# Kernel tuning notes

Measured on AMD Instinct MI355X. Metric: run time of the kernel, lower is better.

The kernel has to match this reference:

```python
import jax, jax.numpy as jnp
import numpy as np

T, R, HEADS, H, L = 4, 8, 4, 128, 2
DK = H // HEADS
NPT = 25000
N = T * NPT
E = 600000
IN_DIMS = [512, 256, 128, 64]


def setup_inputs() -> dict:
    key = jax.random.key(0)
    ks = iter(jax.random.split(key, 64))
    d = {}
    # per-type raw node features (concatenation order = type order)
    for i, di in enumerate(IN_DIMS):
        d[f"nf{i}"] = jax.random.normal(next(ks), (NPT, di), jnp.float32)
    # per-type input encoder MLPs: Linear(di,256) -> ReLU -> Linear(256,H)
    for i, di in enumerate(IN_DIMS):
        d[f"enc_w1_{i}"] = jax.random.normal(next(ks), (di, 256), jnp.float32) * (1.0 / np.sqrt(di))
        d[f"enc_b1_{i}"] = jnp.zeros((256,), jnp.float32)
        d[f"enc_w2_{i}"] = jax.random.normal(next(ks), (256, H), jnp.float32) * (1.0 / np.sqrt(256))
        d[f"enc_b2_{i}"] = jnp.zeros((H,), jnp.float32)
    # HGT conv params, stacked over L layers
    sc = 1.0 / np.sqrt(H)
    for nm in ["Wk", "Wq", "Wv", "Wa"]:
        d[nm] = jax.random.normal(next(ks), (L, T, H, H), jnp.float32) * sc
        d["b" + nm[1]] = jnp.zeros((L, T, H), jnp.float32)
    eye = jnp.broadcast_to(jnp.eye(DK, dtype=jnp.float32), (L, R, HEADS, DK, DK))
    d["rel_att"] = eye + 0.05 * jax.random.normal(next(ks), (L, R, HEADS, DK, DK), jnp.float32)
    d["rel_msg"] = eye + 0.05 * jax.random.normal(next(ks), (L, R, HEADS, DK, DK), jnp.float32)
    d["rel_pri"] = jnp.ones((L, R, HEADS), jnp.float32)
    d["skip"] = jnp.zeros((L, T), jnp.float32)  # sigmoid(0)=0.5 gate
    d["gamma"] = jnp.ones((L, H), jnp.float32)
    d["beta"] = jnp.zeros((L, H), jnp.float32)
    # graph structure
    d["node_types"] = jnp.repeat(jnp.arange(T, dtype=jnp.int32), NPT)
    d["edge_index"] = jax.random.randint(next(ks), (2, E), 0, N, jnp.int32)
    d["edge_types"] = jax.random.randint(next(ks), (E,), 0, R, jnp.int32)
    return d


def typed_linear(x, nt, W, b):
    # W: [T,H,H], b: [T,H]; select per-node-type transform
    allt = jnp.einsum('nd,tdh->tnh', x, W) + b[:, None, :]  # [T,N,H]
    return allt[nt, jnp.arange(x.shape[0])]  # [N,H]


def layer_norm(x, g, b):
    m = x.mean(-1, keepdims=True)
    v = jnp.var(x, -1, keepdims=True)
    return (x - m) * jax.lax.rsqrt(v + 1e-5) * g + b


def hgt_layer(h, nt, src, dst, et, Wk, bk, Wq, bq, Wv, bv, Wa, ba, ra, rm, rp, skip, g, be):
    n = h.shape[0]
    k = typed_linear(h, nt, Wk, bk).reshape(n, HEADS, DK)
    q = typed_linear(h, nt, Wq, bq).reshape(n, HEADS, DK)
    v = typed_linear(h, nt, Wv, bv).reshape(n, HEADS, DK)
    k_s, v_s, q_d = k[src], v[src], q[dst]  # [E,HEADS,DK]
    # relation-conditioned key/message transforms (small fixed loop over R relations)
    kt = jnp.zeros_like(k_s)
    mt = jnp.zeros_like(v_s)
    for r in range(R):
        msk = (et == r)[:, None, None]
        kt = kt + jnp.where(msk, jnp.einsum('ehd,hdf->ehf', k_s, ra[r]), 0.0)
        mt = mt + jnp.where(msk, jnp.einsum('ehd,hdf->ehf', v_s, rm[r]), 0.0)
    att = (q_d * kt).sum(-1) * rp[et] * (1.0 / np.sqrt(DK))  # [E,HEADS]
    # segment softmax over incoming edges of each target node
    amax = jax.ops.segment_max(att, dst, num_segments=n)
    amax = jnp.where(jnp.isfinite(amax), amax, 0.0)
    ea = jnp.exp(att - amax[dst])
    den = jax.ops.segment_sum(ea, dst, num_segments=n)
    w = ea / jnp.maximum(den[dst], 1e-9)
    res = jax.ops.segment_sum(w[:, :, None] * mt, dst, num_segments=n).reshape(n, H)
    trans = typed_linear(jax.nn.gelu(res, approximate=False), nt, Wa, ba)
    alpha = jax.nn.sigmoid(skip)[nt][:, None]
    out = trans * alpha + h * (1.0 - alpha)
    return layer_norm(out, g, be)


def reference(nf0, nf1, nf2, nf3,
              enc_w1_0, enc_b1_0, enc_w2_0, enc_b2_0,
              enc_w1_1, enc_b1_1, enc_w2_1, enc_b2_1,
              enc_w1_2, enc_b1_2, enc_w2_2, enc_b2_2,
              enc_w1_3, enc_b1_3, enc_w2_3, enc_b2_3,
              Wk, bk, Wq, bq, Wv, bv, Wa, ba,
              rel_att, rel_msg, rel_pri, skip, gamma, beta,
              node_types, edge_index, edge_types):
    encs = [(enc_w1_0, enc_b1_0, enc_w2_0, enc_b2_0),
            (enc_w1_1, enc_b1_1, enc_w2_1, enc_b2_1),
            (enc_w1_2, enc_b1_2, enc_w2_2, enc_b2_2),
            (enc_w1_3, enc_b1_3, enc_w2_3, enc_b2_3)]
    embs = [jax.nn.relu(nf @ w1 + b1) @ w2 + b2
            for nf, (w1, b1, w2, b2) in zip([nf0, nf1, nf2, nf3], encs)]
    h = jnp.concatenate(embs, axis=0)  # [N,H]; dropout is identity in eval mode
    src, dst = edge_index[0], edge_index[1]
    for l in range(L):
        h = hgt_layer(h, node_types, src, dst, edge_types,
                      Wk[l], bk[l], Wq[l], bq[l], Wv[l], bv[l], Wa[l], ba[l],
                      rel_att[l], rel_msg[l], rel_pri[l], skip[l], gamma[l], beta[l])
    return h
```

## Files before the change

### kernel.cpp

```cpp
#include <hip/hip_runtime.h>
#include <math.h>


#define NPT   25000
#define NN    100000
#define EE    600000
#define HD    128
#define NRELS 8

typedef unsigned short u16;
typedef unsigned int   u32;
using s16x8 = __attribute__((ext_vector_type(8))) short;
using f32x4 = __attribute__((ext_vector_type(4))) float;

__device__ __forceinline__ u16 f2bf(float x){
  u32 u = __float_as_uint(x);
  u += 0x7fffu + ((u >> 16) & 1u);
  return (u16)(u >> 16);
}
__device__ __forceinline__ float bf2f(u16 v){ return __uint_as_float(((u32)v) << 16); }

struct CastArgs {
  const float* src[12];
  u16* dst[12];
  int K[12], N[12], B[12];
  int blk0[13];
};

__global__ __launch_bounds__(256) void cast_all(CastArgs a){
  int blk = blockIdx.x;
  int s = 0;
  while (s < 11 && blk >= a.blk0[s + 1]) s++;
  long idx = (long)(blk - a.blk0[s]) * 256 + threadIdx.x;
  int K = a.K[s], N = a.N[s];
  long per = (long)K * N;
  long tot = per * a.B[s];
  if (idx >= tot) return;
  int b = (int)(idx / per);
  long rem = idx - (long)b * per;
  int n = (int)(rem / K), k = (int)(rem - (long)n * K);
  a.dst[s][idx] = f2bf(a.src[s][(long)b * per + (long)k * N + n]);
}

__global__ __launch_bounds__(256) void pack_rel(const float* __restrict__ ra,
                                                const float* __restrict__ rm,
                                                u16* __restrict__ out){
  int idx = blockIdx.x * 256 + threadIdx.x;
  if (idx >= 131072) return;
  int j = idx & 7, lane = (idx >> 3) & 63, nc = (idx >> 9) & 1;
  int h = (idx >> 10) & 3, r = (idx >> 12) & 7, mat = (idx >> 15) & 1, l = idx >> 16;
  const float* src = mat ? rm : ra;
  float v = src[(((long)l * 8 + r) * 4 + h) * 1024 + ((lane >> 4) * 8 + j) * 32 + nc * 16 + (lane & 15)];
  out[idx] = f2bf(v);
}

__global__ __launch_bounds__(256) void hist_key(const int* __restrict__ ei,
                                                const int* __restrict__ et,
                                                int* __restrict__ hist){
  int e = blockIdx.x * 256 + threadIdx.x;
  if (e < EE) atomicAdd(&hist[et[e] * NN + ei[EE + e]], 1);
}

__global__ __launch_bounds__(256) void scan_part_g(const int* __restrict__ in,
                                                   int* __restrict__ bsum, int n){
  __shared__ int sh[256];
  int i = blockIdx.x * 256 + threadIdx.x;
  sh[threadIdx.x] = (i < n) ? in[i] : 0;
  __syncthreads();
  for (int s = 128; s > 0; s >>= 1){
    if (threadIdx.x < s) sh[threadIdx.x] += sh[threadIdx.x + s];
    __syncthreads();
  }
  if (threadIdx.x == 0) bsum[blockIdx.x] = sh[0];
}

__global__ __launch_bounds__(512) void scan_bsum(int* bsum, int nb){
  __shared__ int sh[512];
  int t = threadIdx.x;
  int orig = (t < nb) ? bsum[t] : 0;
  sh[t] = orig;
  __syncthreads();
  for (int off = 1; off < 512; off <<= 1){
    int u = (t >= off) ? sh[t - off] : 0;
    __syncthreads();
    sh[t] += u;
    __syncthreads();
  }
  if (t < nb) bsum[t] = sh[t] - orig;
}

__global__ __launch_bounds__(256) void scan_fin_g(const int* __restrict__ in,
                                                  const int* __restrict__ bsum,
                                                  int* __restrict__ out, int n){
  __shared__ int sh[256];
  int i = blockIdx.x * 256 + threadIdx.x;
  int v = (i < n) ? in[i] : 0;
  sh[threadIdx.x] = v;
  __syncthreads();
  for (int off = 1; off < 256; off <<= 1){
    int u = (threadIdx.x >= off) ? sh[threadIdx.x - off] : 0;
    __syncthreads();
    sh[threadIdx.x] += u;
    __syncthreads();
  }
  if (i < n) out[i] = sh[threadIdx.x] - v + bsum[blockIdx.x];
}

__global__ void extract_offs(const int* __restrict__ cur, int* __restrict__ meta){
  int r = threadIdx.x;
  if (r < NRELS) meta[16 + r] = cur[r * NN];
  if (r == 0) meta[24] = EE;
}

__global__ __launch_bounds__(256) void scatter_key(const int* __restrict__ ei,
                                                   const int* __restrict__ et,
                                                   int* __restrict__ cur,
                                                   int* __restrict__ ss, int* __restrict__ sd){
  int e = blockIdx.x * 256 + threadIdx.x;
  if (e < EE){
    int s = ei[e], d = ei[EE + e];
    int p = atomicAdd(&cur[et[e] * NN + d], 1);
    ss[p] = s;
    sd[p] = d;
  }
}

__global__ __launch_bounds__(256) void hist_dst(const int* __restrict__ sd, int* __restrict__ hist){
  int e = blockIdx.x * 256 + threadIdx.x;
  if (e < EE) atomicAdd(&hist[sd[e]], 1);
}

__global__ __launch_bounds__(256) void scan_fin(const int* __restrict__ hist,
                                                const int* __restrict__ bsum,
                                                int* __restrict__ rowp, int* __restrict__ cursor){
  __shared__ int sh[256];
  int i = blockIdx.x * 256 + threadIdx.x;
  int v = (i < NN) ? hist[i] : 0;
  sh[threadIdx.x] = v;
  __syncthreads();
  for (int off = 1; off < 256; off <<= 1){
    int u = (threadIdx.x >= off) ? sh[threadIdx.x - off] : 0;
    __syncthreads();
    sh[threadIdx.x] += u;
    __syncthreads();
  }
  int excl = sh[threadIdx.x] - v + bsum[blockIdx.x];
  if (i < NN){ rowp[i] = excl; cursor[i] = excl; }
  if (i == NN - 1) rowp[NN] = excl + v;
}

__global__ __launch_bounds__(256) void dp_scat(const int* __restrict__ sd,
                                               int* __restrict__ cursor, int* __restrict__ dp){
  int e = blockIdx.x * 256 + threadIdx.x;
  if (e < EE) dp[e] = atomicAdd(&cursor[sd[e]], 1);
}

template<bool A_F32, bool RELU, bool OUTF32, bool OUTBF16>
__global__ __launch_bounds__(256)
void gemm_k(const void* __restrict__ Ap, const u16* __restrict__ Bt,
            const float* __restrict__ bias,
            float* __restrict__ Cf, u16* __restrict__ Cbf,
            int M, int N, int K, int sAr, int sB, int sBias, int sCr,
            int ldC, int colOff)
{
  __shared__ __align__(16) u16 As[128 * 40];
  __shared__ __align__(16) u16 Bs[128 * 40];
  int z = blockIdx.z;
  int tid = threadIdx.x, wv = tid >> 6, lane = tid & 63;
  int m0 = blockIdx.x * 128, n0 = blockIdx.y * 128;
  int wm = (wv >> 1) * 64, wn = (wv & 1) * 64;
  long aBase = (long)z * sAr * K;
  const u16*   Ab  = (const u16*)Ap;
  const float* Afp = (const float*)Ap;
  const u16* Bz = Bt + (long)z * sB;
  const float* biz = bias + (long)z * sBias;
  long cRow0 = (long)z * sCr;
  int r2 = tid >> 1, hf = tid & 1;

  f32x4 acc[4][4];
  #pragma unroll
  for (int i = 0; i < 4; i++)
    #pragma unroll
    for (int j = 0; j < 4; j++) acc[i][j] = (f32x4){0.f, 0.f, 0.f, 0.f};

  for (int kk = 0; kk < K; kk += 32){
    {
      int gm = m0 + r2;
      #pragma unroll
      for (int c = 0; c < 2; c++){
        int ko = kk + c * 16 + hf * 8;
        union { u16 us[8]; uint4 v; } pk;
        if (gm < M){
          if (!A_F32){
            pk.v = *(const uint4*)(Ab + aBase + (long)gm * K + ko);
          } else {
            const float* s = Afp + aBase + (long)gm * K + ko;
            float4 f0 = *(const float4*)s;
            float4 f1 = *(const float4*)(s + 4);
            pk.us[0] = f2bf(f0.x); pk.us[1] = f2bf(f0.y); pk.us[2] = f2bf(f0.z); pk.us[3] = f2bf(f0.w);
            pk.us[4] = f2bf(f1.x); pk.us[5] = f2bf(f1.y); pk.us[6] = f2bf(f1.z); pk.us[7] = f2bf(f1.w);
          }
        } else {
          pk.v = make_uint4(0u, 0u, 0u, 0u);
        }
        *(uint4*)&As[r2 * 40 + c * 16 + hf * 8] = pk.v;
      }
    }
    {
      int gn = n0 + r2;
      #pragma unroll
      for (int c = 0; c < 2; c++){
        int ko = kk + c * 16 + hf * 8;
        uint4 v;
        if (gn < N) v = *(const uint4*)(Bz + (long)gn * K + ko);
        else        v = make_uint4(0u, 0u, 0u, 0u);
        *(uint4*)&Bs[r2 * 40 + c * 16 + hf * 8] = v;
      }
    }
    __syncthreads();
    s16x8 af[4], bfr[4];
    int rr = lane & 15, q8 = (lane >> 4) * 8;
    #pragma unroll
    for (int mt = 0; mt < 4; mt++) af[mt]  = *(const s16x8*)&As[(wm + mt * 16 + rr) * 40 + q8];
    #pragma unroll
    for (int nt = 0; nt < 4; nt++) bfr[nt] = *(const s16x8*)&Bs[(wn + nt * 16 + rr) * 40 + q8];
    #pragma unroll
    for (int mt = 0; mt < 4; mt++)
      #pragma unroll
      for (int nt = 0; nt < 4; nt++)
        acc[mt][nt] = __builtin_amdgcn_mfma_f32_16x16x32_bf16(af[mt], bfr[nt], acc[mt][nt], 0, 0, 0);
    __syncthreads();
  }
  int col = lane & 15, row4 = (lane >> 4) * 4;
  #pragma unroll
  for (int mt = 0; mt < 4; mt++){
    #pragma unroll
    for (int nt = 0; nt < 4; nt++){
      int gn = n0 + wn + nt * 16 + col;
      float bb = (gn < N) ? biz[gn] : 0.f;
      #pragma unroll
      for (int r = 0; r < 4; r++){
        int gm = m0 + wm + mt * 16 + row4 + r;
        if (gm < M && gn < N){
          float vv = acc[mt][nt][r] + bb;
          if (RELU) vv = fmaxf(vv, 0.f);
          long ci = (cRow0 + gm) * (long)ldC + colOff + gn;
          if (OUTF32)  Cf[ci]  = vv;
          if (OUTBF16) Cbf[ci] = f2bf(vv);
        }
      }
    }
  }
}

__global__ __launch_bounds__(256)
void gemm_kvq(const u16* __restrict__ A,
              const u16* __restrict__ BK, const u16* __restrict__ BV, const u16* __restrict__ BQ,
              const float* __restrict__ bK, const float* __restrict__ bV, const float* __restrict__ bQ,
              u16* __restrict__ kvb, u16* __restrict__ qb)
{
  __shared__ __align__(16) u16 As[128 * 40];
  __shared__ __align__(16) u16 Bs[128 * 40];
  int bx = blockIdx.x;
  int grp = bx % 3;
  int m0 = (bx / 3) * 128;
  int z = blockIdx.z;
  int tid = threadIdx.x, wv = tid >> 6, lane = tid & 63;
  int wm = (wv >> 1) * 64, wn = (wv & 1) * 64;
  long aBase = (long)z * NPT * 128;
  const u16* Bz = ((grp == 0) ? BK : (grp == 1) ? BV : BQ) + (long)z * 16384;
  const float* biz = ((grp == 0) ? bK : (grp == 1) ? bV : bQ) + z * 128;
  u16* C = (grp == 2) ? qb : kvb;
  int ldC = (grp == 2) ? 128 : 256;
  int colOff = (grp == 1) ? 128 : 0;
  long cRow0 = (long)z * NPT;
  int r2 = tid >> 1, hf = tid & 1;

  f32x4 acc[4][4];
  #pragma unroll
  for (int i = 0; i < 4; i++)
    #pragma unroll
    for (int j = 0; j < 4; j++) acc[i][j] = (f32x4){0.f, 0.f, 0.f, 0.f};

  for (int kk = 0; kk < 128; kk += 32){
    {
      int gm = m0 + r2;
      #pragma unroll
      for (int c = 0; c < 2; c++){
        int ko = kk + c * 16 + hf * 8;
        uint4 v;
        if (gm < NPT) v = *(const uint4*)(A + aBase + (long)gm * 128 + ko);
        else          v = make_uint4(0u, 0u, 0u, 0u);
        *(uint4*)&As[r2 * 40 + c * 16 + hf * 8] = v;
      }
    }
    {
      int gn = r2;
      #pragma unroll
      for (int c = 0; c < 2; c++){
        int ko = kk + c * 16 + hf * 8;
        uint4 v = *(const uint4*)(Bz + (long)gn * 128 + ko);
        *(uint4*)&Bs[r2 * 40 + c * 16 + hf * 8] = v;
      }
    }
    __syncthreads();
    s16x8 af[4], bfr[4];
    int rr = lane & 15, q8 = (lane >> 4) * 8;
    #pragma unroll
    for (int mt = 0; mt < 4; mt++) af[mt]  = *(const s16x8*)&As[(wm + mt * 16 + rr) * 40 + q8];
    #pragma unroll
    for (int nt = 0; nt < 4; nt++) bfr[nt] = *(const s16x8*)&Bs[(wn + nt * 16 + rr) * 40 + q8];
    #pragma unroll
    for (int mt = 0; mt < 4; mt++)
      #pragma unroll
      for (int nt = 0; nt < 4; nt++)
        acc[mt][nt] = __builtin_amdgcn_mfma_f32_16x16x32_bf16(af[mt], bfr[nt], acc[mt][nt], 0, 0, 0);
    __syncthreads();
  }
  int col = lane & 15, row4 = (lane >> 4) * 4;
  #pragma unroll
  for (int mt = 0; mt < 4; mt++){
    #pragma unroll
    for (int nt = 0; nt < 4; nt++){
      int gn = wn + nt * 16 + col;
      float bb = biz[gn];
      #pragma unroll
      for (int r = 0; r < 4; r++){
        int gm = m0 + wm + mt * 16 + row4 + r;
        if (gm < NPT){
          float vv = acc[mt][nt][r] + bb;
          C[(cRow0 + gm) * (long)ldC + colOff + gn] = f2bf(vv);
        }
      }
    }
  }
}

__global__ __launch_bounds__(256)
void gemm_ln(const u16* __restrict__ A, const u16* __restrict__ Bt,
             const float* __restrict__ bias,
             float* __restrict__ h, u16* __restrict__ hb,
             const float* __restrict__ skl, const float* __restrict__ gmv,
             const float* __restrict__ btv)
{
  __shared__ __align__(16) u16 As[128 * 40];
  __shared__ __align__(16) u16 Bs[128 * 40];
  __shared__ float red[128][4];
  int z = blockIdx.z;
  int tid = threadIdx.x, wv = tid >> 6, lane = tid & 63;
  int m0 = blockIdx.x * 128;
  int wm = (wv >> 1) * 64, wn = (wv & 1) * 64;
  long aBase = (long)z * NPT * 128;
  const u16* Bz = Bt + (long)z * 16384;
  const float* biz = bias + z * 128;
  int r2 = tid >> 1, hf = tid & 1;

  f32x4 acc[4][4];
  #pragma unroll
  for (int i = 0; i < 4; i++)
    #pragma unroll
    for (int j = 0; j < 4; j++) acc[i][j] = (f32x4){0.f, 0.f, 0.f, 0.f};

  for (int kk = 0; kk < 128; kk += 32){
    {
      int gm = m0 + r2;
      #pragma unroll
      for (int c = 0; c < 2; c++){
        int ko = kk + c * 16 + hf * 8;
        uint4 v;
        if (gm < NPT) v = *(const uint4*)(A + aBase + (long)gm * 128 + ko);
        else          v = make_uint4(0u, 0u, 0u, 0u);
        *(uint4*)&As[r2 * 40 + c * 16 + hf * 8] = v;
      }
    }
    {
      int gn = r2;
      #pragma unroll
      for (int c = 0; c < 2; c++){
        int ko = kk + c * 16 + hf * 8;
        uint4 v = *(const uint4*)(Bz + (long)gn * 128 + ko);
        *(uint4*)&Bs[r2 * 40 + c * 16 + hf * 8] = v;
      }
    }
    __syncthreads();
    s16x8 af[4], bfr[4];
    int rr = lane & 15, q8 = (lane >> 4) * 8;
    #pragma unroll
    for (int mt = 0; mt < 4; mt++) af[mt]  = *(const s16x8*)&As[(wm + mt * 16 + rr) * 40 + q8];
    #pragma unroll
    for (int nt = 0; nt < 4; nt++) bfr[nt] = *(const s16x8*)&Bs[(wn + nt * 16 + rr) * 40 + q8];
    #pragma unroll
    for (int mt = 0; mt < 4; mt++)
      #pragma unroll
      for (int nt = 0; nt < 4; nt++)
        acc[mt][nt] = __builtin_amdgcn_mfma_f32_16x16x32_bf16(af[mt], bfr[nt], acc[mt][nt], 0, 0, 0);
    __syncthreads();
  }

  int col = lane & 15, q = lane >> 4, row4 = q * 4;
  float alpha = 1.f / (1.f + __expf(-skl[z]));
  float bb[4], ga[4], be[4];
  #pragma unroll
  for (int nt = 0; nt < 4; nt++){
    int gn = wn + nt * 16 + col;
    bb[nt] = biz[gn];
    ga[nt] = gmv[gn];
    be[nt] = btv[gn];
  }

  #pragma unroll
  for (int mt = 0; mt < 4; mt++){
    #pragma unroll
    for (int rr = 0; rr < 4; rr++){
      int gmr = m0 + wm + mt * 16 + row4 + rr;
      bool ok = gmr < NPT;
      long rb = ((long)z * NPT + gmr) * HD;
      float p1 = 0.f, p2 = 0.f;
      #pragma unroll
      for (int nt = 0; nt < 4; nt++){
        int gn = wn + nt * 16 + col;
        float hv = ok ? h[rb + gn] : 0.f;
        float vf = (acc[mt][nt][rr] + bb[nt]) * alpha + hv * (1.f - alpha);
        acc[mt][nt][rr] = vf;
        p1 += vf;
        p2 += vf * vf;
      }
      #pragma unroll
      for (int mk = 1; mk < 16; mk <<= 1){
        p1 += __shfl_xor(p1, mk);
        p2 += __shfl_xor(p2, mk);
      }
      if (col == 0){
        int lr = wm + mt * 16 + row4 + rr;
        red[lr][2 * (wn >> 6)]     = p1;
        red[lr][2 * (wn >> 6) + 1] = p2;
      }
    }
  }
  __syncthreads();

  #pragma unroll
  for (int mt = 0; mt < 4; mt++){
    #pragma unroll
    for (int rr = 0; rr < 4; rr++){
      int lr = wm + mt * 16 + row4 + rr;
      int gmr = m0 + lr;
      float ts1 = red[lr][0] + red[lr][2];
      float ts2 = red[lr][1] + red[lr][3];
      float mean = ts1 * (1.f / HD);
      float var = ts2 * (1.f / HD) - mean * mean;
      float rstd = rsqrtf(fmaxf(var, 0.f) + 1e-5f);
      if (gmr < NPT){
        long rb = ((long)z * NPT + gmr) * HD;
        #pragma unroll
        for (int nt = 0; nt < 4; nt++){
          int gn = wn + nt * 16 + col;
          float y = (acc[mt][nt][rr] - mean) * rstd * ga[nt] + be[nt];
          h[rb + gn]  = y;
          hb[rb + gn] = f2bf(y);
        }
      }
    }
  }
}

__global__ __launch_bounds__(256)
void edge_fused(const u16* __restrict__ kvb, const u16* __restrict__ qb,
                const int* __restrict__ ss, const int* __restrict__ sd,
                const int* __restrict__ dp, const int* __restrict__ offs,
                const u16* __restrict__ relpk, const float* __restrict__ rp,
                float* __restrict__ att, u16* __restrict__ wt, int l)
{
  __shared__ __align__(16) u16 ktS[4][16][136];
  int r = blockIdx.y;
  int lo = offs[r], hi = offs[r + 1];
  int base = lo + blockIdx.x * 64;
  if (base >= hi) return;
  int cnt = hi - base; if (cnt > 64) cnt = 64;
  int tid = threadIdx.x, wv = tid >> 6, lane = tid & 63;
  if (wv * 16 >= cnt) return;
  int wcnt = cnt - wv * 16; if (wcnt > 16) wcnt = 16;
  int m = lane & 15, g = lane >> 4;
  int ebase = base + wv * 16;

  int mq = lane >> 2, part = lane & 3;
  int mqc = (mq < wcnt) ? mq : (wcnt - 1);
  int dnq = sd[ebase + mqc];
  int dpq = dp[ebase + mqc];
  const u16* qrow = qb + (long)dnq * 128 + part * 32;
  uint4 qv[4];
  #pragma unroll
  for (int j = 0; j < 4; j++) qv[j] = *(const uint4*)(qrow + j * 8);

  int mm = (m < wcnt) ? m : (wcnt - 1);
  int s_ = ss[ebase + mm];
  const u16* krow = kvb + (long)s_ * 256;
  s16x8 ak[4], av[4];
  #pragma unroll
  for (int h = 0; h < 4; h++){
    ak[h] = *(const s16x8*)(krow + h * 32 + g * 8);
    av[h] = *(const s16x8*)(krow + 128 + h * 32 + g * 8);
  }

  const u16* relA = relpk + (((long)l * 2) * 8 + r) * 4096;
  f32x4 tt[4][2];
  #pragma unroll
  for (int h = 0; h < 4; h++)
    #pragma unroll
    for (int nc = 0; nc < 2; nc++){
      s16x8 b = *(const s16x8*)(relA + h * 1024 + nc * 512 + lane * 8);
      tt[h][nc] = __builtin_amdgcn_mfma_f32_16x16x32_bf16(ak[h], b, (f32x4){0.f,0.f,0.f,0.f}, 0, 0, 0);
    }
  int col = lane & 15, row4 = (lane >> 4) * 4;
  #pragma unroll
  for (int h = 0; h < 4; h++)
    #pragma unroll
    for (int nc = 0; nc < 2; nc++)
      #pragma unroll
      for (int rr = 0; rr < 4; rr++)
        ktS[wv][row4 + rr][h * 32 + nc * 16 + col] = f2bf(tt[h][nc][rr]);
  __asm__ volatile("s_waitcnt lgkmcnt(0)" ::: "memory");

  {
    const u16* ktrow = &ktS[wv][mq][part * 32];
    float p = 0.f;
    #pragma unroll
    for (int j = 0; j < 4; j++){
      uint4 kk4 = *(const uint4*)(ktrow + j * 8);
      uint4 qq4 = qv[j];
      const u32* kw = (const u32*)&kk4;
      const u32* qw = (const u32*)&qq4;
      #pragma unroll
      for (int t = 0; t < 4; t++){
        u32 kk = kw[t], qq = qw[t];
        p = fmaf(bf2f((u16)(kk & 0xffffu)), bf2f((u16)(qq & 0xffffu)), p);
        p = fmaf(__uint_as_float(kk & 0xffff0000u), __uint_as_float(qq & 0xffff0000u), p);
      }
    }
    if (mq < wcnt)
      att[(long)dpq * 4 + part] = p * rp[r * 4 + part] * 0.17677669529663689f;
  }
  __asm__ volatile("s_waitcnt lgkmcnt(0)" ::: "memory");

  const u16* relM = relpk + (((long)l * 2 + 1) * 8 + r) * 4096;
  #pragma unroll
  for (int h = 0; h < 4; h++)
    #pragma unroll
    for (int nc = 0; nc < 2; nc++){
      s16x8 b = *(const s16x8*)(relM + h * 1024 + nc * 512 + lane * 8);
      tt[h][nc] = __builtin_amdgcn_mfma_f32_16x16x32_bf16(av[h], b, (f32x4){0.f,0.f,0.f,0.f}, 0, 0, 0);
    }
  #pragma unroll
  for (int h = 0; h < 4; h++)
    #pragma unroll
    for (int nc = 0; nc < 2; nc++)
      #pragma unroll
      for (int rr = 0; rr < 4; rr++)
        ktS[wv][row4 + rr][h * 32 + nc * 16 + col] = f2bf(tt[h][nc][rr]);
  __asm__ volatile("s_waitcnt lgkmcnt(0)" ::: "memory");

  if (mq < wcnt){
    #pragma unroll
    for (int j = 0; j < 4; j++){
      uint4 v = *(const uint4*)&ktS[wv][mq][part * 32 + j * 8];
      *(uint4*)(wt + (long)dpq * 128 + part * 32 + j * 8) = v;
    }
  }
}

__global__ __launch_bounds__(256)
void seg_reduce(const float* __restrict__ att, const u16* __restrict__ wt,
                const int* __restrict__ rowp, u16* __restrict__ gA)
{
  __shared__ __align__(16) float eas[4][64][4];
  int wv = threadIdx.x >> 6, lane = threadIdx.x & 63;
  int d = blockIdx.x * 4 + wv;
  if (d >= NN) return;
  int first = rowp[d], last = rowp[d + 1];
  int hsel = lane >> 4;
  float m0 = -1e30f, m1 = -1e30f, m2 = -1e30f, m3 = -1e30f;
  float den0 = 0, den1 = 0, den2 = 0, den3 = 0;
  float acc0 = 0, acc1 = 0;
  for (int c0 = first; c0 < last; c0 += 64){
    int cnt = min(64, last - c0);
    float4 a;
    if (lane < cnt) a = *(const float4*)(att + (long)(c0 + lane) * 4);
    else            a = make_float4(-1e30f, -1e30f, -1e30f, -1e30f);
    float c_0 = a.x, c_1 = a.y, c_2 = a.z, c_3 = a.w;
    #pragma unroll
    for (int mm = 1; mm < 64; mm <<= 1){
      c_0 = fmaxf(c_0, __shfl_xor(c_0, mm));
      c_1 = fmaxf(c_1, __shfl_xor(c_1, mm));
      c_2 = fmaxf(c_2, __shfl_xor(c_2, mm));
      c_3 = fmaxf(c_3, __shfl_xor(c_3, mm));
    }
    float n0 = fmaxf(m0, c_0), n1 = fmaxf(m1, c_1), n2 = fmaxf(m2, c_2), n3 = fmaxf(m3, c_3);
    float r0 = __expf(m0 - n0), r1 = __expf(m1 - n1), r2 = __expf(m2 - n2), r3 = __expf(m3 - n3);
    den0 *= r0; den1 *= r1; den2 *= r2; den3 *= r3;
    float rsel = (hsel == 0) ? r0 : (hsel == 1) ? r1 : (hsel == 2) ? r2 : r3;
    acc0 *= rsel; acc1 *= rsel;
    m0 = n0; m1 = n1; m2 = n2; m3 = n3;
    float e_0 = 0, e_1 = 0, e_2 = 0, e_3 = 0;
    if (lane < cnt){
      e_0 = __expf(a.x - m0); e_1 = __expf(a.y - m1);
      e_2 = __expf(a.z - m2); e_3 = __expf(a.w - m3);
    }
    float s0 = e_0, s1 = e_1, s2 = e_2, s3 = e_3;
    #pragma unroll
    for (int mm = 1; mm < 64; mm <<= 1){
      s0 += __shfl_xor(s0, mm); s1 += __shfl_xor(s1, mm);
      s2 += __shfl_xor(s2, mm); s3 += __shfl_xor(s3, mm);
    }
    den0 += s0; den1 += s1; den2 += s2; den3 += s3;
    *(float4*)&eas[wv][lane][0] = make_float4(e_0, e_1, e_2, e_3);
    for (int i = 0; i < cnt; i++){
      float ea = eas[wv][i][hsel];
      u32 w = *(const u32*)(wt + (long)(c0 + i) * HD + 2 * lane);
      acc0 = fmaf(ea, bf2f((u16)(w & 0xffffu)), acc0);
      acc1 = fmaf(ea, __uint_as_float(w & 0xffff0000u), acc1);
    }
  }
  float dh = (hsel == 0) ? den0 : (hsel == 1) ? den1 : (hsel == 2) ? den2 : den3;
  float x0 = acc0 / fmaxf(dh, 1e-9f);
  float x1 = acc1 / fmaxf(dh, 1e-9f);
  x0 = 0.5f * x0 * (1.0f + erff(x0 * 0.70710678118654752f));
  x1 = 0.5f * x1 * (1.0f + erff(x1 * 0.70710678118654752f));
  u32 o = (u32)f2bf(x0) | ((u32)f2bf(x1) << 16);
  *(u32*)(gA + (long)d * HD + 2 * lane) = o;
}

extern "C" void kernel_launch(void* const* d_in, const int* in_sizes, int n_in,
                              void* d_out, int out_size, void* d_ws, size_t ws_size,
                              hipStream_t stream)
{
  const float* nf[4]  = {(const float*)d_in[0], (const float*)d_in[1], (const float*)d_in[2], (const float*)d_in[3]};
  const float* ew1[4] = {(const float*)d_in[4], (const float*)d_in[8],  (const float*)d_in[12], (const float*)d_in[16]};
  const float* eb1[4] = {(const float*)d_in[5], (const float*)d_in[9],  (const float*)d_in[13], (const float*)d_in[17]};
  const float* ew2[4] = {(const float*)d_in[6], (const float*)d_in[10], (const float*)d_in[14], (const float*)d_in[18]};
  const float* eb2[4] = {(const float*)d_in[7], (const float*)d_in[11], (const float*)d_in[15], (const float*)d_in[19]};
  const float* Wk = (const float*)d_in[20]; const float* bk = (const float*)d_in[21];
  const float* Wq = (const float*)d_in[22]; const float* bq = (const float*)d_in[23];
  const float* Wv = (const float*)d_in[24]; const float* bv = (const float*)d_in[25];
  const float* Wa = (const float*)d_in[26]; const float* ba = (const float*)d_in[27];
  const float* rel_att = (const float*)d_in[28];
  const float* rel_msg = (const float*)d_in[29];
  const float* rel_pri = (const float*)d_in[30];
  const float* skp = (const float*)d_in[31];
  const float* gma = (const float*)d_in[32];
  const float* bta = (const float*)d_in[33];
  const int* edge_index = (const int*)d_in[35];
  const int* edge_types = (const int*)d_in[36];
  float* out = (float*)d_out;
  char* ws = (char*)d_ws;

  u16*   kvb   = (u16*)  (ws + 0L);
  u16*   qb    = (u16*)  (ws + 51200000L);
  u16*   gA    = (u16*)  (ws + 51200000L);
  u16*   wt    = (u16*)  (ws + 76800000L);
  u16*   hbf   = (u16*)  (ws + 76800000L);
  u16*   hid   = (u16*)  (ws + 102400000L);
  float* attb  = (float*)(ws + 230400000L);
  int*   hist800 = (int*)(ws + 230400000L);
  int*   cur800  = (int*)(ws + 233600128L);
  int*   b1      = (int*)(ws + 236800256L);
  int*   b2      = (int*)(ws + 236816384L);
  int*   bsum    = (int*)(ws + 236816512L);
  int*   ss    = (int*)  (ws + 240000000L);
  int*   sd    = (int*)  (ws + 242400000L);
  int*   dp    = (int*)  (ws + 244800000L);
  int*   rowp  = (int*)  (ws + 247200000L);
  int*   curs  = (int*)  (ws + 247600128L);
  u16*   relpk = (u16*)  (ws + 247600128L);
  int*   meta  = (int*)  (ws + 248000128L);
  u16*   w1t   = (u16*)  (ws + 248000384L);
  u16*   w2t   = (u16*)  (ws + 248491904L);
  u16*   wkt   = (u16*)  (ws + 248754048L);
  u16*   wqt   = (u16*)  (ws + 249016192L);
  u16*   wvt   = (u16*)  (ws + 249278336L);
  u16*   wat   = (u16*)  (ws + 249540480L);

  int  di[4]  = {512, 256, 128, 64};
  long w1o[4] = {0, 131072, 196608, 229376};

  {
    CastArgs ca;
    for (int i = 0; i < 4; i++){
      ca.src[i] = ew1[i]; ca.dst[i] = w1t + w1o[i]; ca.K[i] = di[i]; ca.N[i] = 256; ca.B[i] = 1;
      ca.src[4 + i] = ew2[i]; ca.dst[4 + i] = w2t + (long)i * 32768; ca.K[4 + i] = 256; ca.N[4 + i] = 128; ca.B[4 + i] = 1;
    }
    const float* bigs[4] = {Wk, Wq, Wv, Wa};
    u16* bigd[4] = {wkt, wqt, wvt, wat};
    for (int i = 0; i < 4; i++){
      ca.src[8 + i] = bigs[i]; ca.dst[8 + i] = bigd[i];
      ca.K[8 + i] = 128; ca.N[8 + i] = 128; ca.B[8 + i] = 8;
    }
    int blocks[12] = {512, 256, 128, 64, 128, 128, 128, 128, 512, 512, 512, 512};
    int acc = 0;
    for (int i = 0; i < 12; i++){ ca.blk0[i] = acc; acc += blocks[i]; }
    ca.blk0[12] = acc;
    cast_all<<<acc, 256, 0, stream>>>(ca);
  }

  hipMemsetAsync(hist800, 0, 3200000, stream);
  hist_key   <<<2344, 256, 0, stream>>>(edge_index, edge_types, hist800);
  scan_part_g<<<3125, 256, 0, stream>>>(hist800, b1, 800000);
  scan_part_g<<<13,   256, 0, stream>>>(b1, b2, 3125);
  scan_bsum  <<<1,    512, 0, stream>>>(b2, 13);
  scan_fin_g <<<13,   256, 0, stream>>>(b1, b2, b1, 3125);
  scan_fin_g <<<3125, 256, 0, stream>>>(hist800, b1, cur800, 800000);
  extract_offs<<<1, 64, 0, stream>>>(cur800, meta);
  scatter_key<<<2344, 256, 0, stream>>>(edge_index, edge_types, cur800, ss, sd);

  hipMemsetAsync(curs, 0, 400000, stream);
  hist_dst   <<<2344, 256, 0, stream>>>(sd, curs);
  scan_part_g<<<391, 256, 0, stream>>>(curs, bsum, NN);
  scan_bsum  <<<1, 512, 0, stream>>>(bsum, 391);
  scan_fin   <<<391, 256, 0, stream>>>(curs, bsum, rowp, curs);
  dp_scat    <<<2344, 256, 0, stream>>>(sd, curs, dp);

  pack_rel<<<512, 256, 0, stream>>>(rel_att, rel_msg, relpk);

  for (int i = 0; i < 4; i++){
    gemm_k<true,  true,  false, true><<<dim3(196, 2, 1), 256, 0, stream>>>(
        nf[i], w1t + w1o[i], eb1[i], nullptr, hid, NPT, 256, di[i], 0, 0, 0, 0, 256, 0);
    gemm_k<false, false, true,  true><<<dim3(196, 1, 1), 256, 0, stream>>>(
        hid, w2t + (long)i * 32768, eb2[i],
        out + (long)i * NPT * HD, hbf + (long)i * NPT * HD, NPT, 128, 256, 0, 0, 0, 0, 128, 0);
  }

  for (int l = 0; l < 2; l++){
    gemm_kvq<<<dim3(588, 1, 4), 256, 0, stream>>>(
        hbf, wkt + (long)l * 65536, wvt + (long)l * 65536, wqt + (long)l * 65536,
        bk + l * 512, bv + l * 512, bq + l * 512, kvb, qb);

    edge_fused<<<dim3(1200, 8), 256, 0, stream>>>(
        kvb, qb, ss, sd, dp, meta + 16, relpk, rel_pri + l * 32, attb, wt, l);

    seg_reduce<<<25000, 256, 0, stream>>>(attb, wt, rowp, gA);

    gemm_ln<<<dim3(196, 1, 4), 256, 0, stream>>>(
        gA, wat + (long)l * 65536, ba + l * 512, out, hbf,
        skp + l * 4, gma + l * 128, bta + l * 128);
  }
}
```

Measured before the change: 1.111 ms.

## Batch encoder GEMMs across types and give each destination node a quarter-wave in seg_reduce

The eight per-type encoder GEMM launches become two launches that index the node type through blockIdx.z. Each type's hidden activations now go to its own slice of the hid buffer, which requires that buffer to hold four types at once. seg_reduce now assigns 16 lanes per destination node instead of a whole 64-lane wave, with each lane handling 8 channels through uint4 loads; this targets idle lanes at the low average in-degree. The running-max rescaling of the softmax is removed and raw exp is used. That is cheaper, but it risks overflow if attention logits get large.

```diff
diff --git a/kernel.cpp b/kernel.cpp
--- a/kernel.cpp
+++ b/kernel.cpp
@@ -155,26 +155,26 @@
   if (e < EE) dp[e] = atomicAdd(&cursor[sd[e]], 1);
 }
 
-template<bool A_F32, bool RELU, bool OUTF32, bool OUTBF16>
+struct Enc1Args {
+  const float* A[4];
+  const float* bias[4];
+  long boff[4];
+  int K[4];
+};
+
 __global__ __launch_bounds__(256)
-void gemm_k(const void* __restrict__ Ap, const u16* __restrict__ Bt,
-            const float* __restrict__ bias,
-            float* __restrict__ Cf, u16* __restrict__ Cbf,
-            int M, int N, int K, int sAr, int sB, int sBias, int sCr,
-            int ldC, int colOff)
+void gemm_enc1(Enc1Args ea, const u16* __restrict__ w1t, u16* __restrict__ hid)
 {
   __shared__ __align__(16) u16 As[128 * 40];
   __shared__ __align__(16) u16 Bs[128 * 40];
   int z = blockIdx.z;
+  int K = ea.K[z];
+  const float* Afp = ea.A[z];
+  const u16* Bz = w1t + ea.boff[z];
+  const float* biz = ea.bias[z];
   int tid = threadIdx.x, wv = tid >> 6, lane = tid & 63;
   int m0 = blockIdx.x * 128, n0 = blockIdx.y * 128;
   int wm = (wv >> 1) * 64, wn = (wv & 1) * 64;
-  long aBase = (long)z * sAr * K;
-  const u16*   Ab  = (const u16*)Ap;
-  const float* Afp = (const float*)Ap;
-  const u16* Bz = Bt + (long)z * sB;
-  const float* biz = bias + (long)z * sBias;
-  long cRow0 = (long)z * sCr;
   int r2 = tid >> 1, hf = tid & 1;
 
   f32x4 acc[4][4];
@@ -190,16 +190,12 @@
       for (int c = 0; c < 2; c++){
         int ko = kk + c * 16 + hf * 8;
         union { u16 us[8]; uint4 v; } pk;
-        if (gm < M){
-          if (!A_F32){
-            pk.v = *(const uint4*)(Ab + aBase + (long)gm * K + ko);
-          } else {
-            const float* s = Afp + aBase + (long)gm * K + ko;
-            float4 f0 = *(const float4*)s;
-            float4 f1 = *(const float4*)(s + 4);
-            pk.us[0] = f2bf(f0.x); pk.us[1] = f2bf(f0.y); pk.us[2] = f2bf(f0.z); pk.us[3] = f2bf(f0.w);
-            pk.us[4] = f2bf(f1.x); pk.us[5] = f2bf(f1.y); pk.us[6] = f2bf(f1.z); pk.us[7] = f2bf(f1.w);
-          }
+        if (gm < NPT){
+          const float* s = Afp + (long)gm * K + ko;
+          float4 f0 = *(const float4*)s;
+          float4 f1 = *(const float4*)(s + 4);
+          pk.us[0] = f2bf(f0.x); pk.us[1] = f2bf(f0.y); pk.us[2] = f2bf(f0.z); pk.us[3] = f2bf(f0.w);
+          pk.us[4] = f2bf(f1.x); pk.us[5] = f2bf(f1.y); pk.us[6] = f2bf(f1.z); pk.us[7] = f2bf(f1.w);
         } else {
           pk.v = make_uint4(0u, 0u, 0u, 0u);
         }
@@ -211,9 +207,7 @@
       #pragma unroll
       for (int c = 0; c < 2; c++){
         int ko = kk + c * 16 + hf * 8;
-        uint4 v;
-        if (gn < N) v = *(const uint4*)(Bz + (long)gn * K + ko);
-        else        v = make_uint4(0u, 0u, 0u, 0u);
+        uint4 v = *(const uint4*)(Bz + (long)gn * K + ko);
         *(uint4*)&Bs[r2 * 40 + c * 16 + hf * 8] = v;
       }
     }
@@ -237,16 +231,92 @@
     #pragma unroll
     for (int nt = 0; nt < 4; nt++){
       int gn = n0 + wn + nt * 16 + col;
-      float bb = (gn < N) ? biz[gn] : 0.f;
+      float bb = biz[gn];
       #pragma unroll
       for (int r = 0; r < 4; r++){
         int gm = m0 + wm + mt * 16 + row4 + r;
-        if (gm < M && gn < N){
+        if (gm < NPT){
+          float vv = fmaxf(acc[mt][nt][r] + bb, 0.f);
+          hid[((long)z * NPT + gm) * 256 + gn] = f2bf(vv);
+        }
+      }
+    }
+  }
+}
+
+struct Enc2Args { const float* bias[4]; };
+
+__global__ __launch_bounds__(256)
+void gemm_enc2(Enc2Args eb, const u16* __restrict__ hid, const u16* __restrict__ w2t,
+               float* __restrict__ outp, u16* __restrict__ hbf)
+{
+  __shared__ __align__(16) u16 As[128 * 40];
+  __shared__ __align__(16) u16 Bs[128 * 40];
+  int z = blockIdx.z;
+  const u16* A = hid + (long)z * NPT * 256;
+  const u16* Bz = w2t + (long)z * 32768;
+  const float* biz = eb.bias[z];
+  int tid = threadIdx.x, wv = tid >> 6, lane = tid & 63;
+  int m0 = blockIdx.x * 128;
+  int wm = (wv >> 1) * 64, wn = (wv & 1) * 64;
+  int r2 = tid >> 1, hf = tid & 1;
+
+  f32x4 acc[4][4];
+  #pragma unroll
+  for (int i = 0; i < 4; i++)
+    #pragma unroll
+    for (int j = 0; j < 4; j++) acc[i][j] = (f32x4){0.f, 0.f, 0.f, 0.f};
+
+  for (int kk = 0; kk < 256; kk += 32){
+    {
+      int gm = m0 + r2;
+      #pragma unroll
+      for (int c = 0; c < 2; c++){
+        int ko = kk + c * 16 + hf * 8;
+        uint4 v;
+        if (gm < NPT) v = *(const uint4*)(A + (long)gm * 256 + ko);
+        else          v = make_uint4(0u, 0u, 0u, 0u);
+        *(uint4*)&As[r2 * 40 + c * 16 + hf * 8] = v;
+      }
+    }
+    {
+      int gn = r2;
+      #pragma unroll
+      for (int c = 0; c < 2; c++){
+        int ko = kk + c * 16 + hf * 8;
+        uint4 v = *(const uint4*)(Bz + (long)gn * 256 + ko);
+        *(uint4*)&Bs[r2 * 40 + c * 16 + hf * 8] = v;
+      }
+    }
+    __syncthreads();
+    s16x8 af[4], bfr[4];
+    int rr = lane & 15, q8 = (lane >> 4) * 8;
+    #pragma unroll
+    for (int mt = 0; mt < 4; mt++) af[mt]  = *(const s16x8*)&As[(wm + mt * 16 + rr) * 40 + q8];
+    #pragma unroll
+    for (int nt = 0; nt < 4; nt++) bfr[nt] = *(const s16x8*)&Bs[(wn + nt * 16 + rr) * 40 + q8];
+    #pragma unroll
+    for (int mt = 0; mt < 4; mt++)
+      #pragma unroll
+      for (int nt = 0; nt < 4; nt++)
+        acc[mt][nt] = __builtin_amdgcn_mfma_f32_16x16x32_bf16(af[mt], bfr[nt], acc[mt][nt], 0, 0, 0);
+    __syncthreads();
+  }
+  int col = lane & 15, row4 = (lane >> 4) * 4;
+  #pragma unroll
+  for (int mt = 0; mt < 4; mt++){
+    #pragma unroll
+    for (int nt = 0; nt < 4; nt++){
+      int gn = wn + nt * 16 + col;
+      float bb = biz[gn];
+      #pragma unroll
+      for (int r = 0; r < 4; r++){
+        int gm = m0 + wm + mt * 16 + row4 + r;
+        if (gm < NPT){
           float vv = acc[mt][nt][r] + bb;
-          if (RELU) vv = fmaxf(vv, 0.f);
-          long ci = (cRow0 + gm) * (long)ldC + colOff + gn;
-          if (OUTF32)  Cf[ci]  = vv;
-          if (OUTBF16) Cbf[ci] = f2bf(vv);
+          long ci = ((long)z * NPT + gm) * (long)HD + gn;
+          outp[ci] = vv;
+          hbf[ci]  = f2bf(vv);
         }
       }
     }
@@ -572,61 +642,56 @@
 void seg_reduce(const float* __restrict__ att, const u16* __restrict__ wt,
                 const int* __restrict__ rowp, u16* __restrict__ gA)
 {
-  __shared__ __align__(16) float eas[4][64][4];
+  __shared__ float eas[4][4][16][4];
   int wv = threadIdx.x >> 6, lane = threadIdx.x & 63;
-  int d = blockIdx.x * 4 + wv;
+  int grp = lane >> 4, il = lane & 15;
+  int d = blockIdx.x * 16 + wv * 4 + grp;
   if (d >= NN) return;
   int first = rowp[d], last = rowp[d + 1];
-  int hsel = lane >> 4;
-  float m0 = -1e30f, m1 = -1e30f, m2 = -1e30f, m3 = -1e30f;
-  float den0 = 0, den1 = 0, den2 = 0, den3 = 0;
-  float acc0 = 0, acc1 = 0;
-  for (int c0 = first; c0 < last; c0 += 64){
-    int cnt = min(64, last - c0);
-    float4 a;
-    if (lane < cnt) a = *(const float4*)(att + (long)(c0 + lane) * 4);
-    else            a = make_float4(-1e30f, -1e30f, -1e30f, -1e30f);
-    float c_0 = a.x, c_1 = a.y, c_2 = a.z, c_3 = a.w;
-    #pragma unroll
-    for (int mm = 1; mm < 64; mm <<= 1){
-      c_0 = fmaxf(c_0, __shfl_xor(c_0, mm));
-      c_1 = fmaxf(c_1, __shfl_xor(c_1, mm));
-      c_2 = fmaxf(c_2, __shfl_xor(c_2, mm));
-      c_3 = fmaxf(c_3, __shfl_xor(c_3, mm));
-    }
-    float n0 = fmaxf(m0, c_0), n1 = fmaxf(m1, c_1), n2 = fmaxf(m2, c_2), n3 = fmaxf(m3, c_3);
-    float r0 = __expf(m0 - n0), r1 = __expf(m1 - n1), r2 = __expf(m2 - n2), r3 = __expf(m3 - n3);
-    den0 *= r0; den1 *= r1; den2 *= r2; den3 *= r3;
-    float rsel = (hsel == 0) ? r0 : (hsel == 1) ? r1 : (hsel == 2) ? r2 : r3;
-    acc0 *= rsel; acc1 *= rsel;
-    m0 = n0; m1 = n1; m2 = n2; m3 = n3;
+  int head = il >> 2;
+  float den0 = 0.f, den1 = 0.f, den2 = 0.f, den3 = 0.f;
+  float a0 = 0, a1 = 0, a2 = 0, a3 = 0, a4 = 0, a5 = 0, a6 = 0, a7 = 0;
+  for (int c0 = first; c0 < last; c0 += 16){
+    int cnt = min(16, last - c0);
     float e_0 = 0, e_1 = 0, e_2 = 0, e_3 = 0;
-    if (lane < cnt){
-      e_0 = __expf(a.x - m0); e_1 = __expf(a.y - m1);
-      e_2 = __expf(a.z - m2); e_3 = __expf(a.w - m3);
+    if (il < cnt){
+      float4 a = *(const float4*)(att + (long)(c0 + il) * 4);
+      e_0 = __expf(a.x); e_1 = __expf(a.y); e_2 = __expf(a.z); e_3 = __expf(a.w);
     }
     float s0 = e_0, s1 = e_1, s2 = e_2, s3 = e_3;
     #pragma unroll
-    for (int mm = 1; mm < 64; mm <<= 1){
-      s0 += __shfl_xor(s0, mm); s1 += __shfl_xor(s1, mm);
-      s2 += __shfl_xor(s2, mm); s3 += __shfl_xor(s3, mm);
+    for (int mk = 1; mk < 16; mk <<= 1){
+      s0 += __shfl_xor(s0, mk); s1 += __shfl_xor(s1, mk);
+      s2 += __shfl_xor(s2, mk); s3 += __shfl_xor(s3, mk);
     }
     den0 += s0; den1 += s1; den2 += s2; den3 += s3;
-    *(float4*)&eas[wv][lane][0] = make_float4(e_0, e_1, e_2, e_3);
+    *(float4*)&eas[wv][grp][il][0] = make_float4(e_0, e_1, e_2, e_3);
     for (int i = 0; i < cnt; i++){
-      float ea = eas[wv][i][hsel];
-      u32 w = *(const u32*)(wt + (long)(c0 + i) * HD + 2 * lane);
-      acc0 = fmaf(ea, bf2f((u16)(w & 0xffffu)), acc0);
-      acc1 = fmaf(ea, __uint_as_float(w & 0xffff0000u), acc1);
-    }
-  }
-  float dh = (hsel == 0) ? den0 : (hsel == 1) ? den1 : (hsel == 2) ? den2 : den3;
-  float x0 = acc0 / fmaxf(dh, 1e-9f);
-  float x1 = acc1 / fmaxf(dh, 1e-9f);
-  x0 = 0.5f * x0 * (1.0f + erff(x0 * 0.70710678118654752f));
-  x1 = 0.5f * x1 * (1.0f + erff(x1 * 0.70710678118654752f));
-  u32 o = (u32)f2bf(x0) | ((u32)f2bf(x1) << 16);
-  *(u32*)(gA + (long)d * HD + 2 * lane) = o;
+      float ea = eas[wv][grp][i][head];
+      uint4 w = *(const uint4*)(wt + (long)(c0 + i) * HD + il * 8);
+      a0 = fmaf(ea, bf2f((u16)(w.x & 0xffffu)), a0);
+      a1 = fmaf(ea, __uint_as_float(w.x & 0xffff0000u), a1);
+      a2 = fmaf(ea, bf2f((u16)(w.y & 0xffffu)), a2);
+      a3 = fmaf(ea, __uint_as_float(w.y & 0xffff0000u), a3);
+      a4 = fmaf(ea, bf2f((u16)(w.z & 0xffffu)), a4);
+      a5 = fmaf(ea, __uint_as_float(w.z & 0xffff0000u), a5);
+      a6 = fmaf(ea, bf2f((u16)(w.w & 0xffffu)), a6);
+      a7 = fmaf(ea, __uint_as_float(w.w & 0xffff0000u), a7);
+    }
+  }
+  float dh = (head == 0) ? den0 : (head == 1) ? den1 : (head == 2) ? den2 : den3;
+  float inv = 1.f / fmaxf(dh, 1e-9f);
+  float x[8] = {a0 * inv, a1 * inv, a2 * inv, a3 * inv,
+                a4 * inv, a5 * inv, a6 * inv, a7 * inv};
+  u32 o[4];
+  #pragma unroll
+  for (int j = 0; j < 4; j++){
+    float y0 = x[2 * j], y1 = x[2 * j + 1];
+    y0 = 0.5f * y0 * (1.0f + erff(y0 * 0.70710678118654752f));
+    y1 = 0.5f * y1 * (1.0f + erff(y1 * 0.70710678118654752f));
+    o[j] = (u32)f2bf(y0) | ((u32)f2bf(y1) << 16);
+  }
+  *(uint4*)(gA + (long)d * HD + il * 8) = make_uint4(o[0], o[1], o[2], o[3]);
 }
 
 extern "C" void kernel_launch(void* const* d_in, const int* in_sizes, int n_in,
@@ -720,12 +785,15 @@
 
   pack_rel<<<512, 256, 0, stream>>>(rel_att, rel_msg, relpk);
 
-  for (int i = 0; i < 4; i++){
-    gemm_k<true,  true,  false, true><<<dim3(196, 2, 1), 256, 0, stream>>>(
-        nf[i], w1t + w1o[i], eb1[i], nullptr, hid, NPT, 256, di[i], 0, 0, 0, 0, 256, 0);
-    gemm_k<false, false, true,  true><<<dim3(196, 1, 1), 256, 0, stream>>>(
-        hid, w2t + (long)i * 32768, eb2[i],
-        out + (long)i * NPT * HD, hbf + (long)i * NPT * HD, NPT, 128, 256, 0, 0, 0, 0, 128, 0);
+  {
+    Enc1Args e1;
+    for (int i = 0; i < 4; i++){
+      e1.A[i] = nf[i]; e1.bias[i] = eb1[i]; e1.boff[i] = w1o[i]; e1.K[i] = di[i];
+    }
+    gemm_enc1<<<dim3(196, 2, 4), 256, 0, stream>>>(e1, w1t, hid);
+    Enc2Args e2;
+    for (int i = 0; i < 4; i++) e2.bias[i] = eb2[i];
+    gemm_enc2<<<dim3(196, 1, 4), 256, 0, stream>>>(e2, hid, w2t, out, hbf);
   }
 
   for (int l = 0; l < 2; l++){
@@ -736,7 +804,7 @@
     edge_fused<<<dim3(1200, 8), 256, 0, stream>>>(
         kvb, qb, ss, sd, dp, meta + 16, relpk, rel_pri + l * 32, attb, wt, l);
 
-    seg_reduce<<<25000, 256, 0, stream>>>(attb, wt, rowp, gA);
+    seg_reduce<<<6250, 256, 0, stream>>>(attb, wt, rowp, gA);
 
     gemm_ln<<<dim3(196, 1, 4), 256, 0, stream>>>(
         gA, wat + (long)l * 65536, ba + l * 512, out, hbf,
```

Result: faster. 969.7 us (-12.7%).
